# Kernel optimization log

Measured on AMD Instinct MI355X. Metric: run time of the kernel, lower is better.

## Reference

```python
import jax, jax.numpy as jnp
import numpy as np

H_RATIO = 0.33  # matches init_kwargs h_ratio
EPS = 1e-12     # F.normalize default eps


def setup_inputs() -> dict:
    key = jax.random.key(0)
    x = jax.random.normal(key, (64, 2048, 24, 12), dtype=jnp.float32)
    return {"x": x}


def reference(x):
    b, c, h, w = x.shape
    rh = round(H_RATIO * h)  # number of top-energy rows to drop (static)
    # per-sample spatial activation energy, summed over channels: (b, h*w)
    act = jnp.sum(x * x, axis=1).reshape(b, h * w)
    # L2 normalize per sample (faithful to F.normalize; order-preserving anyway)
    norm = jnp.sqrt(jnp.sum(act * act, axis=1, keepdims=True))
    act = act / jnp.maximum(norm, EPS)
    act = act.reshape(b, h, w)
    # per-row max over width -> (b, h); take indices of the rh largest rows
    max_act = jnp.max(act, axis=2)
    ind = jnp.argsort(max_act, axis=1)[:, -rh:]  # (b, rh)
    # row mask: ones everywhere, zero at the top-rh rows per sample
    mask = jnp.ones((b, h), dtype=x.dtype)
    mask = mask.at[jnp.arange(b)[:, None], ind].set(0.0)  # (b, h)
    # broadcast over channels and width (equiv. to the repeat_interleave chain)
    return x * mask[:, None, :, None]
```

## Files before the change

### kernel.cpp

```cpp
#include <hip/hip_runtime.h>

#define B   64
#define C   2048
#define H   24
#define W   12
#define S   (H * W)
#define S4  (S / 4)
#define W4  (W / 4)
#define NCH 32
#define CCH (C / NCH)
#define RH  8

typedef float f4 __attribute__((ext_vector_type(4)));

__global__ __launch_bounds__(288) void k_energy(const float* __restrict__ x,
                                                float* __restrict__ part) {
    const int chunk = blockIdx.x;
    const int b     = blockIdx.y;
    const int t     = threadIdx.x;
    const int f     = t % S4;
    const int g     = t / S4;

    const f4* __restrict__ x4 =
        (const f4*)x + (size_t)(b * C + chunk * CCH) * S4;

    f4 acc = {0.f, 0.f, 0.f, 0.f};
    #pragma unroll
    for (int k = 0; k < CCH / 4; ++k) {
        f4 v = x4[t + S * k];
        acc += v * v;
    }

    __shared__ f4 sm4[4][S4];
    sm4[g][f] = acc;
    __syncthreads();

    const float* sm = (const float*)sm4;
    part[((size_t)b * NCH + chunk) * S + t] =
        sm[0 * S + t] + sm[1 * S + t] + sm[2 * S + t] + sm[3 * S + t];
}

__global__ __launch_bounds__(288) void k_select(const float* __restrict__ part,
                                                int* __restrict__ drop) {
    const int b = blockIdx.x;
    const int t = threadIdx.x;

    __shared__ float act[S];
    __shared__ float rm[H];

    const float* p = part + (size_t)b * NCH * S + t;
    float sum = 0.f;
    #pragma unroll
    for (int ch = 0; ch < NCH; ch++) sum += p[(size_t)ch * S];
    act[t] = sum;
    __syncthreads();

    if (t < H) {
        float m = act[t * W];
        #pragma unroll
        for (int w = 1; w < W; w++) m = fmaxf(m, act[t * W + w]);
        rm[t] = m;
    }
    __syncthreads();

    if (t < H) {
        const float mt = rm[t];
        int cnt = 0;
        #pragma unroll
        for (int j = 0; j < H; j++) {
            float mj = rm[j];
            if (mj > mt || (mj == mt && j > t)) cnt++;
        }
        drop[b * H + t] = (cnt < RH) ? 1 : 0;
    }
}

__global__ __launch_bounds__(288) void k_mask_copy(const float* __restrict__ x,
                                                   float* __restrict__ out,
                                                   const int* __restrict__ drop) {
    const int chunk = blockIdx.x;
    const int b     = blockIdx.y;
    const int t     = threadIdx.x;
    const int h     = (t % S4) / W4;
    const float keep = (drop[b * H + h] == 0) ? 1.0f : 0.0f;

    const size_t base4 = (size_t)(b * C + chunk * CCH) * S4;
    const f4* __restrict__ x4 = (const f4*)x + base4;
    f4* __restrict__       o4 = (f4*)out + base4;

    #pragma unroll
    for (int k = 0; k < CCH / 4; ++k) {
        f4 v = x4[t + S * k];
        f4 r = v * keep;
        __builtin_nontemporal_store(r, &o4[t + S * k]);
    }
}

extern "C" void kernel_launch(void* const* d_in, const int* in_sizes, int n_in,
                              void* d_out, int out_size, void* d_ws, size_t ws_size,
                              hipStream_t stream) {
    const float* x   = (const float*)d_in[0];
    float*       out = (float*)d_out;

    float* part = (float*)d_ws;
    int*   drop = (int*)((char*)d_ws + (size_t)B * NCH * S * sizeof(float));

    k_energy<<<dim3(NCH, B), 288, 0, stream>>>(x, part);
    k_select<<<B, 288, 0, stream>>>(part, drop);
    k_mask_copy<<<dim3(NCH, B), 288, 0, stream>>>(x, out, drop);
}
```

Baseline: 278.3 us.

## Fuse energy, selection and masked copy into one kernel with per-sample flags

Merges the three kernels into a single kernel. Each block loads its slice of x into registers, writes partial energies, and counts arrivals per sample with an atomic. The last block to arrive for a sample computes the drop mask and publishes it through a ready flag; all blocks spin on that flag, then write the masked output from the values still in registers. This removes the second full read of x and two kernel launches. In exchange it relies on inter-block spin-waiting, which can deadlock if a sample's blocks are not all resident at once, and it adds a small init kernel.

```diff
diff --git a/kernel.cpp b/kernel.cpp
--- a/kernel.cpp
+++ b/kernel.cpp
@@ -1,98 +1,124 @@
 #include <hip/hip_runtime.h>
 
-#define B   64
-#define C   2048
-#define H   24
-#define W   12
-#define S   (H * W)
-#define S4  (S / 4)
-#define W4  (W / 4)
-#define NCH 32
-#define CCH (C / NCH)
-#define RH  8
+#define B    64
+#define C    2048
+#define H    24
+#define W    12
+#define S    288
+#define S4   72
+#define W4   3
+#define NCH  32
+#define CCH  64
+#define RH   8
+#define T    576
+#define G    8
+#define KPT  8
 
 typedef float f4 __attribute__((ext_vector_type(4)));
 
-__global__ __launch_bounds__(288) void k_energy(const float* __restrict__ x,
-                                                float* __restrict__ part) {
+__global__ __launch_bounds__(128) void k_init(unsigned int* flags) {
+    flags[threadIdx.x] = 0u;
+}
+
+__global__ __launch_bounds__(T) void k_fused(const float* __restrict__ x,
+                                             float* __restrict__ out,
+                                             float* __restrict__ part,
+                                             unsigned int* __restrict__ cnt,
+                                             unsigned int* __restrict__ ready) {
     const int chunk = blockIdx.x;
-    const int b     = blockIdx.y;
+    const int s     = blockIdx.y;
     const int t     = threadIdx.x;
     const int f     = t % S4;
     const int g     = t / S4;
 
-    const f4* __restrict__ x4 =
-        (const f4*)x + (size_t)(b * C + chunk * CCH) * S4;
+    const size_t base4 = (size_t)(s * C + chunk * CCH) * S4;
+    const f4* __restrict__ x4 = (const f4*)x + base4;
+    f4* __restrict__       o4 = (f4*)out + base4;
 
+    f4 v[KPT];
     f4 acc = {0.f, 0.f, 0.f, 0.f};
     #pragma unroll
-    for (int k = 0; k < CCH / 4; ++k) {
-        f4 v = x4[t + S * k];
-        acc += v * v;
+    for (int k = 0; k < KPT; ++k) {
+        v[k] = x4[t + T * k];
+        acc += v[k] * v[k];
     }
 
-    __shared__ f4 sm4[4][S4];
-    sm4[g][f] = acc;
+    __shared__ f4 sm[G][S4];
+    __shared__ unsigned int lmask;
+    __shared__ int lastflag;
+    sm[g][f] = acc;
     __syncthreads();
 
-    const float* sm = (const float*)sm4;
-    part[((size_t)b * NCH + chunk) * S + t] =
-        sm[0 * S + t] + sm[1 * S + t] + sm[2 * S + t] + sm[3 * S + t];
-}
-
-__global__ __launch_bounds__(288) void k_select(const float* __restrict__ part,
-                                                int* __restrict__ drop) {
-    const int b = blockIdx.x;
-    const int t = threadIdx.x;
-
-    __shared__ float act[S];
-    __shared__ float rm[H];
-
-    const float* p = part + (size_t)b * NCH * S + t;
-    float sum = 0.f;
-    #pragma unroll
-    for (int ch = 0; ch < NCH; ch++) sum += p[(size_t)ch * S];
-    act[t] = sum;
+    if (t < S) {
+        const float* smf = (const float*)sm;
+        float sum = 0.f;
+        #pragma unroll
+        for (int gg = 0; gg < G; ++gg) sum += smf[gg * S + t];
+        part[((size_t)s * NCH + chunk) * S + t] = sum;
+    }
+    __threadfence();
     __syncthreads();
-
-    if (t < H) {
-        float m = act[t * W];
-        #pragma unroll
-        for (int w = 1; w < W; w++) m = fmaxf(m, act[t * W + w]);
-        rm[t] = m;
+    if (t == 0) {
+        unsigned int old = __hip_atomic_fetch_add(
+            &cnt[s], 1u, __ATOMIC_ACQ_REL, __HIP_MEMORY_SCOPE_AGENT);
+        lastflag = (old == NCH - 1);
     }
     __syncthreads();
 
-    if (t < H) {
-        const float mt = rm[t];
-        int cnt = 0;
-        #pragma unroll
-        for (int j = 0; j < H; j++) {
-            float mj = rm[j];
-            if (mj > mt || (mj == mt && j > t)) cnt++;
+    if (lastflag) {
+        __shared__ float act[S];
+        __shared__ float rm[H];
+        __shared__ unsigned int dropbits;
+        if (t == 0) dropbits = 0u;
+        __syncthreads();
+        if (t < S) {
+            const float* p = part + (size_t)s * NCH * S + t;
+            float sum = 0.f;
+            #pragma unroll
+            for (int ch = 0; ch < NCH; ++ch) sum += p[ch * S];
+            act[t] = sum;
         }
-        drop[b * H + t] = (cnt < RH) ? 1 : 0;
+        __syncthreads();
+        if (t < H) {
+            float m = act[t * W];
+            #pragma unroll
+            for (int w = 1; w < W; ++w) m = fmaxf(m, act[t * W + w]);
+            rm[t] = m;
+        }
+        __syncthreads();
+        if (t < H) {
+            const float mt = rm[t];
+            int bigger = 0;
+            #pragma unroll
+            for (int j = 0; j < H; ++j) {
+                float mj = rm[j];
+                if (mj > mt || (mj == mt && j > t)) bigger++;
+            }
+            if (bigger < RH) atomicOr(&dropbits, 1u << t);
+        }
+        __syncthreads();
+        if (t == 0) {
+            __hip_atomic_store(&ready[s], 0x80000000u | dropbits,
+                               __ATOMIC_RELEASE, __HIP_MEMORY_SCOPE_AGENT);
+        }
     }
-}
 
-__global__ __launch_bounds__(288) void k_mask_copy(const float* __restrict__ x,
-                                                   float* __restrict__ out,
-                                                   const int* __restrict__ drop) {
-    const int chunk = blockIdx.x;
-    const int b     = blockIdx.y;
-    const int t     = threadIdx.x;
-    const int h     = (t % S4) / W4;
-    const float keep = (drop[b * H + h] == 0) ? 1.0f : 0.0f;
+    if (t == 0) {
+        unsigned int word;
+        while ((word = __hip_atomic_load(&ready[s], __ATOMIC_ACQUIRE,
+                                         __HIP_MEMORY_SCOPE_AGENT)) == 0u)
+            __builtin_amdgcn_s_sleep(32);
+        lmask = word;
+    }
+    __syncthreads();
+    const unsigned int mask = lmask;
 
-    const size_t base4 = (size_t)(b * C + chunk * CCH) * S4;
-    const f4* __restrict__ x4 = (const f4*)x + base4;
-    f4* __restrict__       o4 = (f4*)out + base4;
-
+    const int h = f / W4;
+    const float keep = ((mask >> h) & 1u) ? 0.f : 1.f;
     #pragma unroll
-    for (int k = 0; k < CCH / 4; ++k) {
-        f4 v = x4[t + S * k];
-        f4 r = v * keep;
-        __builtin_nontemporal_store(r, &o4[t + S * k]);
+    for (int k = 0; k < KPT; ++k) {
+        f4 r = v[k] * keep;
+        __builtin_nontemporal_store(r, &o4[t + T * k]);
     }
 }
 
@@ -102,10 +128,11 @@
     const float* x   = (const float*)d_in[0];
     float*       out = (float*)d_out;
 
-    float* part = (float*)d_ws;
-    int*   drop = (int*)((char*)d_ws + (size_t)B * NCH * S * sizeof(float));
+    float*        part  = (float*)d_ws;
+    unsigned int* flags = (unsigned int*)((char*)d_ws + (size_t)B * NCH * S * sizeof(float));
+    unsigned int* cnt   = flags;
+    unsigned int* ready = flags + B;
 
-    k_energy<<<dim3(NCH, B), 288, 0, stream>>>(x, part);
-    k_select<<<B, 288, 0, stream>>>(part, drop);
-    k_mask_copy<<<dim3(NCH, B), 288, 0, stream>>>(x, out, drop);
+    k_init<<<1, 128, 0, stream>>>(flags);
+    k_fused<<<dim3(NCH, B), T, 0, stream>>>(x, out, part, cnt, ready);
 }
```

Measured after the change: 968.1 us. 248% more time.
